# Optimization experiments

Measured on AMD Instinct MI355X. Metric: run time of the kernel, lower is better.

## Reference

```python
import jax, jax.numpy as jnp
import numpy as np

B, A, N, E, H, OUT = 32, 16, 10000, 256, 256, 2

def setup_inputs() -> dict:
    key = jax.random.key(0)
    k1, k2, k3, k4, k5, k6 = jax.random.split(key, 6)
    abs_actions = jax.random.normal(k1, (B, A), dtype=jnp.float32)
    assignments = jax.random.randint(k2, (B, N), 0, A, dtype=jnp.int64)
    emb = jax.random.normal(k3, (N, E), dtype=jnp.float32)  # ground_agent_embedding.weight
    s1 = 1.0 / np.sqrt(1 + E)
    W1 = jax.random.uniform(k4, (1 + E, H), jnp.float32, -s1, s1)
    b1 = jnp.zeros((H,), jnp.float32)
    s2 = 1.0 / np.sqrt(H)
    W2 = jax.random.uniform(k5, (H, OUT), jnp.float32, -s2, s2)
    b2 = jnp.zeros((OUT,), jnp.float32)
    return {"abs_actions": abs_actions, "abstract_agent_assignments": assignments,
            "emb": emb, "W1": W1, "b1": b1, "W2": W2, "b2": b2}

def reference(abs_actions, abstract_agent_assignments, emb, W1, b1, W2, b2):
    # per-batch gather: assigned[b, n] = abs_actions[b, assignments[b, n]]  -> (B, N)
    assigned = jnp.take_along_axis(abs_actions, abstract_agent_assignments, axis=1)
    # concat scalar action with broadcast embedding table -> (B, N, 1+E)
    x = jnp.concatenate(
        [assigned[..., None], jnp.broadcast_to(emb[None], (assigned.shape[0],) + emb.shape)],
        axis=-1)
    # shared small MLP (MultiChannelNet, n_channels=1): Linear -> ReLU -> Linear
    h = jax.nn.relu(jnp.einsum("bnf,fh->bnh", x, W1) + b1)
    return jnp.einsum("bnh,ho->bno", h, W2) + b2  # (B, N, OUT) action logits
```

## Files before the change

### kernel.cpp

```cpp
#include <hip/hip_runtime.h>


constexpr int B_ = 32, A_ = 16, N_ = 10000, E_ = 256, H_ = 256;
constexpr int TN = 16, NBLK = N_ / TN;

typedef __attribute__((ext_vector_type(8))) short bf16x8;
typedef __attribute__((ext_vector_type(4))) float f32x4;

__device__ __align__(16) ushort g_w1t[H_ * E_];

static __device__ __forceinline__ ushort f2bf(float x) {
    union { float f; unsigned u; } c; c.f = x;
    unsigned r = c.u + 0x7fff + ((c.u >> 16) & 1);
    return (ushort)(r >> 16);
}

__global__ __launch_bounds__(256, 1) void prep_w1t_k(const float* __restrict__ W1) {
    __shared__ float tile[64][65];
    const int bk = blockIdx.x >> 2, bh = blockIdx.x & 3;
    const int tx = threadIdx.x & 63, ty = threadIdx.x >> 6;
    #pragma unroll
    for (int kk = ty; kk < 64; kk += 4)
        tile[kk][tx] = W1[(size_t)(1 + bk * 64 + kk) * H_ + bh * 64 + tx];
    __syncthreads();
    #pragma unroll
    for (int hh = ty; hh < 64; hh += 4)
        g_w1t[(size_t)(bh * 64 + hh) * E_ + bk * 64 + tx] = f2bf(tile[tx][hh]);
}

__global__ __launch_bounds__(256, 2) void decoder_main(
    const float* __restrict__ abs_actions,
    const int*   __restrict__ asgn,
    const float* __restrict__ emb,
    const float* __restrict__ W1,
    const float* __restrict__ b1,
    const float* __restrict__ W2,
    const float* __restrict__ b2,
    float* __restrict__ out)
{
    __shared__ ushort eb[TN * 264];
    __shared__ float  u[TN * 260];
    __shared__ float  vals[B_ * 17];
    __shared__ float  w1r[H_];
    __shared__ float  w2s[2 * H_];

    const int t  = threadIdx.x;
    const int n0 = blockIdx.x * TN;

    #pragma unroll
    for (int q = 0; q < 2; ++q) {
        const int p = t + 256 * q, b = p >> 4, n = p & 15;
        vals[b * 17 + n] = abs_actions[b * A_ + asgn[(size_t)b * N_ + n0 + n]];
    }

    {
        const int row = t >> 4, col = (t & 15) << 4;
        const float4* src = reinterpret_cast<const float4*>(emb + (size_t)(n0 + row) * E_ + col);
        const float4 q0 = src[0], q1 = src[1], q2 = src[2], q3 = src[3];
        union { ushort us[16]; bf16x8 v[2]; } pk;
        const float f[16] = {q0.x,q0.y,q0.z,q0.w, q1.x,q1.y,q1.z,q1.w,
                             q2.x,q2.y,q2.z,q2.w, q3.x,q3.y,q3.z,q3.w};
        #pragma unroll
        for (int i = 0; i < 16; ++i) pk.us[i] = f2bf(f[i]);
        bf16x8* dst = reinterpret_cast<bf16x8*>(&eb[row * 264 + col]);
        dst[0] = pk.v[0]; dst[1] = pk.v[1];
    }
    w1r[t]       = W1[t];
    w2s[t]       = W2[t];
    w2s[256 + t] = W2[256 + t];
    __syncthreads();

    {
        const int lane = t & 63, w = t >> 6;
        const int lr = lane & 15;
        const int lk = (lane >> 4) << 3;
        f32x4 acc[4];
        #pragma unroll
        for (int ct = 0; ct < 4; ++ct) {
            const float bv = b1[w * 64 + ct * 16 + lr];
            acc[ct] = (f32x4){bv, bv, bv, bv};
        }
        #pragma unroll
        for (int ks = 0; ks < 8; ++ks) {
            const bf16x8 af = *reinterpret_cast<const bf16x8*>(&eb[lr * 264 + ks * 32 + lk]);
            #pragma unroll
            for (int ct = 0; ct < 4; ++ct) {
                const bf16x8 bfv = *reinterpret_cast<const bf16x8*>(
                    &g_w1t[(size_t)(w * 64 + ct * 16 + lr) * E_ + ks * 32 + lk]);
                acc[ct] = __builtin_amdgcn_mfma_f32_16x16x32_bf16(af, bfv, acc[ct], 0, 0, 0);
            }
        }
        #pragma unroll
        for (int ct = 0; ct < 4; ++ct)
            #pragma unroll
            for (int r = 0; r < 4; ++r)
                u[((lane >> 4) * 4 + r) * 260 + w * 64 + ct * 16 + lr] = acc[ct][r];
    }
    __syncthreads();

    {
        const float2 b2v = { b2[0], b2[1] };
        float oacc[2][2];
        int   pnn[2], pbb[2];
        float pv[2];
        #pragma unroll
        for (int q = 0; q < 2; ++q) {
            const int p = t + 256 * q, b = p >> 4, n = p & 15;
            pbb[q] = b; pnn[q] = n;
            pv[q] = vals[b * 17 + n];
            oacc[q][0] = 0.f; oacc[q][1] = 0.f;
        }

        #pragma unroll 2
        for (int h = 0; h < 256; h += 4) {
            const float4 wv = *reinterpret_cast<const float4*>(&w1r[h]);
            const float4 p0 = *reinterpret_cast<const float4*>(&w2s[2 * h]);
            const float4 p1 = *reinterpret_cast<const float4*>(&w2s[2 * h + 4]);
            #pragma unroll
            for (int q = 0; q < 2; ++q) {
                const float4 c = *reinterpret_cast<const float4*>(&u[pnn[q] * 260 + h]);
                const float v = pv[q];
                const float t0 = fmaxf(fmaf(v, wv.x, c.x), 0.f);
                const float t1 = fmaxf(fmaf(v, wv.y, c.y), 0.f);
                const float t2 = fmaxf(fmaf(v, wv.z, c.z), 0.f);
                const float t3 = fmaxf(fmaf(v, wv.w, c.w), 0.f);
                oacc[q][0] = fmaf(t0, p0.x, oacc[q][0]);
                oacc[q][1] = fmaf(t0, p0.y, oacc[q][1]);
                oacc[q][0] = fmaf(t1, p0.z, oacc[q][0]);
                oacc[q][1] = fmaf(t1, p0.w, oacc[q][1]);
                oacc[q][0] = fmaf(t2, p1.x, oacc[q][0]);
                oacc[q][1] = fmaf(t2, p1.y, oacc[q][1]);
                oacc[q][0] = fmaf(t3, p1.z, oacc[q][0]);
                oacc[q][1] = fmaf(t3, p1.w, oacc[q][1]);
            }
        }

        #pragma unroll
        for (int q = 0; q < 2; ++q) {
            float2 o; o.x = oacc[q][0] + b2v.x; o.y = oacc[q][1] + b2v.y;
            *reinterpret_cast<float2*>(out + ((size_t)pbb[q] * N_ + n0 + pnn[q]) * 2) = o;
        }
    }
}

extern "C" void kernel_launch(void* const* d_in, const int* in_sizes, int n_in,
                              void* d_out, int out_size, void* d_ws, size_t ws_size,
                              hipStream_t stream) {
    const float* abs_actions = (const float*)d_in[0];
    const int*   asgn        = (const int*)d_in[1];
    const float* emb         = (const float*)d_in[2];
    const float* W1          = (const float*)d_in[3];
    const float* b1          = (const float*)d_in[4];
    const float* W2          = (const float*)d_in[5];
    const float* b2          = (const float*)d_in[6];
    float*       out         = (float*)d_out;

    prep_w1t_k<<<16, 256, 0, stream>>>(W1);
    decoder_main<<<NBLK, 256, 0, stream>>>(abs_actions, asgn, emb, W1, b1, W2, b2, out);
}
```

Baseline: 30.61 us.

## Compute second MLP layer with bf16 MFMA instead of scalar FMAs

Replaces the per-thread scalar FMA loop of the second layer (ReLU hidden times W2) with bf16 MFMA 16x16x32 instructions. W2 is padded to 16 columns, only 2 of which are nonzero, and each lane builds ReLU activations in registers and packs them to bf16. This is meant to offload the dominant ALU work to matrix cores, but it wastes 14/16 of MFMA output columns, adds conversion cost, and lowers precision of the hidden activations. The output stores become strided scalar writes from only 2 of every 16 lanes.

```diff
diff --git a/kernel.cpp b/kernel.cpp
--- a/kernel.cpp
+++ b/kernel.cpp
@@ -1,4 +1,5 @@
 #include <hip/hip_runtime.h>
+#include <hip/hip_bf16.h>
 
 
 constexpr int B_ = 32, A_ = 16, N_ = 10000, E_ = 256, H_ = 256;
@@ -13,6 +14,12 @@
     union { float f; unsigned u; } c; c.f = x;
     unsigned r = c.u + 0x7fff + ((c.u >> 16) & 1);
     return (ushort)(r >> 16);
+}
+
+static __device__ __forceinline__ ushort2 pk2(float lo, float hi) {
+    union { __hip_bfloat162 h; ushort2 u; } c;
+    c.h = __float22bfloat162_rn(float2{lo, hi});
+    return c.u;
 }
 
 __global__ __launch_bounds__(256, 1) void prep_w1t_k(const float* __restrict__ W1) {
@@ -99,46 +106,74 @@
     __syncthreads();
 
     {
-        const float2 b2v = { b2[0], b2[1] };
-        float oacc[2][2];
-        int   pnn[2], pbb[2];
-        float pv[2];
+        const int lane = t & 63, w = t >> 6;
+        const int lr  = lane & 15;
+        const int klo = lane >> 4;
+        const int wn0 = w * 4;
+
+        bf16x8 w2f[8];
         #pragma unroll
-        for (int q = 0; q < 2; ++q) {
-            const int p = t + 256 * q, b = p >> 4, n = p & 15;
-            pbb[q] = b; pnn[q] = n;
-            pv[q] = vals[b * 17 + n];
-            oacc[q][0] = 0.f; oacc[q][1] = 0.f;
+        for (int ks = 0; ks < 8; ++ks) {
+            union { ushort us[8]; bf16x8 v; } pk;
+            #pragma unroll
+            for (int j = 0; j < 8; ++j) {
+                const int h = ks * 32 + klo * 8 + j;
+                pk.us[j] = (lr < 2) ? f2bf(w2s[h * 2 + lr]) : (ushort)0;
+            }
+            w2f[ks] = pk.v;
         }
 
-        #pragma unroll 2
-        for (int h = 0; h < 256; h += 4) {
-            const float4 wv = *reinterpret_cast<const float4*>(&w1r[h]);
-            const float4 p0 = *reinterpret_cast<const float4*>(&w2s[2 * h]);
-            const float4 p1 = *reinterpret_cast<const float4*>(&w2s[2 * h + 4]);
+        float vv[4][2];
+        #pragma unroll
+        for (int n = 0; n < 4; ++n)
             #pragma unroll
-            for (int q = 0; q < 2; ++q) {
-                const float4 c = *reinterpret_cast<const float4*>(&u[pnn[q] * 260 + h]);
-                const float v = pv[q];
-                const float t0 = fmaxf(fmaf(v, wv.x, c.x), 0.f);
-                const float t1 = fmaxf(fmaf(v, wv.y, c.y), 0.f);
-                const float t2 = fmaxf(fmaf(v, wv.z, c.z), 0.f);
-                const float t3 = fmaxf(fmaf(v, wv.w, c.w), 0.f);
-                oacc[q][0] = fmaf(t0, p0.x, oacc[q][0]);
-                oacc[q][1] = fmaf(t0, p0.y, oacc[q][1]);
-                oacc[q][0] = fmaf(t1, p0.z, oacc[q][0]);
-                oacc[q][1] = fmaf(t1, p0.w, oacc[q][1]);
-                oacc[q][0] = fmaf(t2, p1.x, oacc[q][0]);
-                oacc[q][1] = fmaf(t2, p1.y, oacc[q][1]);
-                oacc[q][0] = fmaf(t3, p1.z, oacc[q][0]);
-                oacc[q][1] = fmaf(t3, p1.w, oacc[q][1]);
+            for (int bh = 0; bh < 2; ++bh)
+                vv[n][bh] = vals[(bh * 16 + lr) * 17 + wn0 + n];
+
+        f32x4 acc[4][2] = {};
+
+        #pragma unroll
+        for (int ks = 0; ks < 8; ++ks) {
+            const int k0 = ks * 32 + klo * 8;
+            const float4 wv0 = *reinterpret_cast<const float4*>(&w1r[k0]);
+            const float4 wv1 = *reinterpret_cast<const float4*>(&w1r[k0 + 4]);
+            #pragma unroll
+            for (int n = 0; n < 4; ++n) {
+                const float4 u0 = *reinterpret_cast<const float4*>(&u[(wn0 + n) * 260 + k0]);
+                const float4 u1 = *reinterpret_cast<const float4*>(&u[(wn0 + n) * 260 + k0 + 4]);
+                #pragma unroll
+                for (int bh = 0; bh < 2; ++bh) {
+                    const float v = vv[n][bh];
+                    const float p0 = fmaxf(fmaf(v, wv0.x, u0.x), 0.f);
+                    const float p1 = fmaxf(fmaf(v, wv0.y, u0.y), 0.f);
+                    const float p2 = fmaxf(fmaf(v, wv0.z, u0.z), 0.f);
+                    const float p3 = fmaxf(fmaf(v, wv0.w, u0.w), 0.f);
+                    const float p4 = fmaxf(fmaf(v, wv1.x, u1.x), 0.f);
+                    const float p5 = fmaxf(fmaf(v, wv1.y, u1.y), 0.f);
+                    const float p6 = fmaxf(fmaf(v, wv1.z, u1.z), 0.f);
+                    const float p7 = fmaxf(fmaf(v, wv1.w, u1.w), 0.f);
+                    union { ushort2 u2[4]; bf16x8 v8; } pa;
+                    pa.u2[0] = pk2(p0, p1);
+                    pa.u2[1] = pk2(p2, p3);
+                    pa.u2[2] = pk2(p4, p5);
+                    pa.u2[3] = pk2(p6, p7);
+                    acc[n][bh] = __builtin_amdgcn_mfma_f32_16x16x32_bf16(
+                        pa.v8, w2f[ks], acc[n][bh], 0, 0, 0);
+                }
             }
         }
 
-        #pragma unroll
-        for (int q = 0; q < 2; ++q) {
-            float2 o; o.x = oacc[q][0] + b2v.x; o.y = oacc[q][1] + b2v.y;
-            *reinterpret_cast<float2*>(out + ((size_t)pbb[q] * N_ + n0 + pnn[q]) * 2) = o;
+        if (lr < 2) {
+            const float b2o = b2[lr];
+            #pragma unroll
+            for (int n = 0; n < 4; ++n)
+                #pragma unroll
+                for (int bh = 0; bh < 2; ++bh)
+                    #pragma unroll
+                    for (int r = 0; r < 4; ++r) {
+                        const int b = bh * 16 + klo * 4 + r;
+                        out[((size_t)b * N_ + n0 + wn0 + n) * 2 + lr] = acc[n][bh][r] + b2o;
+                    }
         }
     }
 }
```

New measurement: 34.53 us. +12.8%, slower.

## Compute MLP epilogue in one wave with 8 batches per thread

Applied to the files above, without the earlier changes.

Restricts the relu/second-layer epilogue to the first wave, with each thread handling one node row across 8 batches so the per-node hidden row is loaded from LDS once and reused. Raises the launch-bounds occupancy hint from 2 to 4 blocks per CU. This cuts redundant LDS traffic but puts the epilogue arithmetic on a quarter of the threads, lengthening each block's serial tail, and the occupancy hint may constrain registers.

```diff
diff --git a/kernel.cpp b/kernel.cpp
--- a/kernel.cpp
+++ b/kernel.cpp
@@ -28,7 +28,7 @@
         g_w1t[(size_t)(bh * 64 + hh) * E_ + bk * 64 + tx] = f2bf(tile[tx][hh]);
 }
 
-__global__ __launch_bounds__(256, 2) void decoder_main(
+__global__ __launch_bounds__(256, 4) void decoder_main(
     const float* __restrict__ abs_actions,
     const int*   __restrict__ asgn,
     const float* __restrict__ emb,
@@ -98,47 +98,47 @@
     }
     __syncthreads();
 
-    {
-        const float2 b2v = { b2[0], b2[1] };
-        float oacc[2][2];
-        int   pnn[2], pbb[2];
-        float pv[2];
+    if (t < 64) {
+        const int n  = t & 15;
+        const int bg = t >> 4;
+        const float b20 = b2[0], b21 = b2[1];
+        float vv[8], o0[8], o1[8];
         #pragma unroll
-        for (int q = 0; q < 2; ++q) {
-            const int p = t + 256 * q, b = p >> 4, n = p & 15;
-            pbb[q] = b; pnn[q] = n;
-            pv[q] = vals[b * 17 + n];
-            oacc[q][0] = 0.f; oacc[q][1] = 0.f;
+        for (int bi = 0; bi < 8; ++bi) {
+            vv[bi] = vals[(bg * 8 + bi) * 17 + n];
+            o0[bi] = 0.f; o1[bi] = 0.f;
         }
 
+        const float* br = &u[n * 260];
         #pragma unroll 2
         for (int h = 0; h < 256; h += 4) {
+            const float4 c  = *reinterpret_cast<const float4*>(&br[h]);
             const float4 wv = *reinterpret_cast<const float4*>(&w1r[h]);
             const float4 p0 = *reinterpret_cast<const float4*>(&w2s[2 * h]);
             const float4 p1 = *reinterpret_cast<const float4*>(&w2s[2 * h + 4]);
             #pragma unroll
-            for (int q = 0; q < 2; ++q) {
-                const float4 c = *reinterpret_cast<const float4*>(&u[pnn[q] * 260 + h]);
-                const float v = pv[q];
-                const float t0 = fmaxf(fmaf(v, wv.x, c.x), 0.f);
-                const float t1 = fmaxf(fmaf(v, wv.y, c.y), 0.f);
-                const float t2 = fmaxf(fmaf(v, wv.z, c.z), 0.f);
-                const float t3 = fmaxf(fmaf(v, wv.w, c.w), 0.f);
-                oacc[q][0] = fmaf(t0, p0.x, oacc[q][0]);
-                oacc[q][1] = fmaf(t0, p0.y, oacc[q][1]);
-                oacc[q][0] = fmaf(t1, p0.z, oacc[q][0]);
-                oacc[q][1] = fmaf(t1, p0.w, oacc[q][1]);
-                oacc[q][0] = fmaf(t2, p1.x, oacc[q][0]);
-                oacc[q][1] = fmaf(t2, p1.y, oacc[q][1]);
-                oacc[q][0] = fmaf(t3, p1.z, oacc[q][0]);
-                oacc[q][1] = fmaf(t3, p1.w, oacc[q][1]);
+            for (int bi = 0; bi < 8; ++bi) {
+                const float v = vv[bi];
+                const float r0 = fmaxf(fmaf(v, wv.x, c.x), 0.f);
+                const float r1 = fmaxf(fmaf(v, wv.y, c.y), 0.f);
+                const float r2 = fmaxf(fmaf(v, wv.z, c.z), 0.f);
+                const float r3 = fmaxf(fmaf(v, wv.w, c.w), 0.f);
+                o0[bi] = fmaf(r0, p0.x, o0[bi]);
+                o1[bi] = fmaf(r0, p0.y, o1[bi]);
+                o0[bi] = fmaf(r1, p0.z, o0[bi]);
+                o1[bi] = fmaf(r1, p0.w, o1[bi]);
+                o0[bi] = fmaf(r2, p1.x, o0[bi]);
+                o1[bi] = fmaf(r2, p1.y, o1[bi]);
+                o0[bi] = fmaf(r3, p1.z, o0[bi]);
+                o1[bi] = fmaf(r3, p1.w, o1[bi]);
             }
         }
 
         #pragma unroll
-        for (int q = 0; q < 2; ++q) {
-            float2 o; o.x = oacc[q][0] + b2v.x; o.y = oacc[q][1] + b2v.y;
-            *reinterpret_cast<float2*>(out + ((size_t)pbb[q] * N_ + n0 + pnn[q]) * 2) = o;
+        for (int bi = 0; bi < 8; ++bi) {
+            const int b = bg * 8 + bi;
+            float2 o; o.x = o0[bi] + b20; o.y = o1[bi] + b21;
+            *reinterpret_cast<float2*>(out + ((size_t)b * N_ + n0 + n) * 2) = o;
         }
     }
 }
```

New measurement: 36.40 us. 18.9% more time.
